# Kernel tuning notes

Hardware: AMD Instinct MI355X
Metric: run time of the kernel (lower is better)

The kernel has to match this reference:

```python
import jax, jax.numpy as jnp
import numpy as np

DIM = 256
HEADS = 4
HEAD_DIM = DIM // HEADS
SCALE = HEAD_DIM ** -0.5


def setup_inputs() -> dict:
    key = jax.random.key(0)
    ks = jax.random.split(key, 6)
    B, N, C = 4, 4096, DIM
    x = jax.random.normal(ks[0], (B, N, C), dtype=jnp.float32)
    # torch.nn.Linear weights are [out, in]; y = x @ W.T (+ b)
    s = 1.0 / np.sqrt(C)
    Wq = jax.random.uniform(ks[1], (C, C), jnp.float32, -s, s)
    Wk = jax.random.uniform(ks[2], (C, C), jnp.float32, -s, s)
    Wv = jax.random.uniform(ks[3], (C, C), jnp.float32, -s, s)
    Wp = jax.random.uniform(ks[4], (C, C), jnp.float32, -s, s)
    bp = jax.random.uniform(ks[5], (C,), jnp.float32, -s, s)
    return {"x": x, "Wq": Wq, "Wk": Wk, "Wv": Wv, "Wp": Wp, "bp": bp}


def reference(x, Wq, Wk, Wv, Wp, bp):
    B, N, C = x.shape
    H, D = HEADS, HEAD_DIM
    # project and split heads: [B, H, N, D]
    def heads(W):
        return (x @ W.T).reshape(B, N, H, D).transpose(0, 2, 1, 3)
    q = heads(Wq)
    k = heads(Wk)
    v = heads(Wv)
    attn = jnp.einsum('bhnd,bhmd->bhnm', q, k) * SCALE  # [B,H,N,N]
    attn = jax.nn.softmax(attn, axis=-1)
    out = jnp.einsum('bhnm,bhmd->bhnd', attn, v)  # [B,H,N,D]
    out = out.transpose(0, 2, 1, 3).reshape(B, N, C)
    return out @ Wp.T + bp
```

## Files before the change

kernel.cpp:

```cpp
#include <hip/hip_runtime.h>

typedef unsigned short u16t;
typedef unsigned int u32t;
typedef __bf16 bf16x8 __attribute__((ext_vector_type(8)));
typedef float f32x4 __attribute__((ext_vector_type(4)));
typedef float f32x16 __attribute__((ext_vector_type(16)));
typedef unsigned int u32x4 __attribute__((ext_vector_type(4)));
typedef unsigned int u32x2 __attribute__((ext_vector_type(2)));

#define DEV static __device__ __forceinline__

DEV u16t f2bf(float f){
  u32t u = __builtin_bit_cast(u32t, f);
  u += 0x7fffu + ((u >> 16) & 1u);
  return (u16t)(u >> 16);
}

DEV u32t cvtpk(float lo, float hi){
  u32t r;
  asm("v_cvt_pk_bf16_f32 %0, %1, %2" : "=v"(r) : "v"(lo), "v"(hi));
  return r;
}

DEV void plswap(u32t &a, u32t &b){
  asm("v_permlane32_swap_b32 %0, %1" : "+v"(a), "+v"(b));
}

DEV float fexp2(float x){
#if __has_builtin(__builtin_amdgcn_exp2f)
  return __builtin_amdgcn_exp2f(x);
#else
  return exp2f(x);
#endif
}

DEV void gll16(const void* g, void* l){
  __builtin_amdgcn_global_load_lds((const __attribute__((address_space(1))) void*)g,
                                   (__attribute__((address_space(3))) void*)l, 16, 0, 0);
}

DEV f32x4 mfma16(bf16x8 a, bf16x8 b, f32x4 c){
  return __builtin_amdgcn_mfma_f32_16x16x32_bf16(a, b, c, 0, 0, 0);
}

DEV f32x16 mfma32(bf16x8 a, bf16x8 b, f32x16 c){
  return __builtin_amdgcn_mfma_f32_32x32x16_bf16(a, b, c, 0, 0, 0);
}

__global__ __launch_bounds__(256) void k_cast_x(const float4* __restrict__ x, u16t* __restrict__ xb){
  int idx = blockIdx.x * 256 + threadIdx.x;
  float4 v = x[idx];
  ushort4 o = make_ushort4(f2bf(v.x), f2bf(v.y), f2bf(v.z), f2bf(v.w));
  *(ushort4*)&xb[idx * 4] = o;
}

__global__ __launch_bounds__(256) void k_cast_w(const float* __restrict__ Wq, const float* __restrict__ Wk,
                         const float* __restrict__ Wv, const float* __restrict__ Wp,
                         u16t* __restrict__ wqkv, u16t* __restrict__ wp){
  int idx = blockIdx.x * 256 + threadIdx.x;
  if (idx < 196608){
    float v;
    if (idx < 65536)        v = Wq[idx] * 0.1803368801f;
    else if (idx < 131072)  v = Wk[idx - 65536];
    else                    v = Wv[idx - 131072];
    wqkv[idx] = f2bf(v);
  } else {
    int j = idx - 196608;
    wp[j] = f2bf(Wp[j]);
  }
}

template<bool IS_QKV>
__global__ __launch_bounds__(256) void k_gemm(const u16t* __restrict__ A, const u16t* __restrict__ W,
    const float* __restrict__ bias, u16t* __restrict__ oq, u16t* __restrict__ okk, u16t* __restrict__ vtg,
    float* __restrict__ op, int Ntot){
  __shared__ u32x4 sm[1536];
  const int tid = threadIdx.x, lane = tid & 63, w = tid >> 6, g = lane >> 4, li = lane & 15;
  const int m0 = blockIdx.x * 128, n0 = blockIdx.y * 64;
  const int wm = w >> 1, wn = w & 1;
  f32x4 acc[4][2] = {};
  for (int kk = 0; kk < 4; ++kk){
    #pragma unroll
    for (int rnd = 0; rnd < 4; ++rnd){
      int cid = rnd * 256 + tid;
      int row = cid >> 3, ch = cid & 7;
      const u16t* src = A + (m0 + row) * 256 + kk * 64 + ((ch ^ (row & 7)) << 3);
      gll16(src, (char*)sm + (rnd * 256 + w * 64) * 16);
    }
    #pragma unroll
    for (int rnd = 0; rnd < 2; ++rnd){
      int cid = rnd * 256 + tid;
      int row = cid >> 3, ch = cid & 7;
      const u16t* src = W + (n0 + row) * 256 + kk * 64 + ((ch ^ (row & 7)) << 3);
      gll16(src, (char*)sm + 16384 + (rnd * 256 + w * 64) * 16);
    }
    __syncthreads();
    #pragma unroll
    for (int ks = 0; ks < 2; ++ks){
      bf16x8 bfr[2];
      #pragma unroll
      for (int nj = 0; nj < 2; ++nj){
        int row = wn * 32 + nj * 16 + li;
        bfr[nj] = __builtin_bit_cast(bf16x8, sm[1024 + row * 8 + ((ks * 4 + g) ^ (row & 7))]);
      }
      #pragma unroll
      for (int mi = 0; mi < 4; ++mi){
        int row = wm * 64 + mi * 16 + li;
        bf16x8 af = __builtin_bit_cast(bf16x8, sm[row * 8 + ((ks * 4 + g) ^ (row & 7))]);
        #pragma unroll
        for (int nj = 0; nj < 2; ++nj)
          acc[mi][nj] = mfma16(af, bfr[nj], acc[mi][nj]);
      }
    }
    __syncthreads();
  }
  if (IS_QKV){
    const int which = n0 >> 8, h = (n0 >> 6) & 3;
    if (which == 2){
      u16t* smv = (u16t*)sm;
      #pragma unroll
      for (int mi = 0; mi < 4; ++mi){
        #pragma unroll
        for (int nj = 0; nj < 2; ++nj){
          int d = wn * 32 + nj * 16 + li;
          int mloc = wm * 64 + mi * 16 + g * 4;
          u32x2 pk2;
          pk2.x = cvtpk(acc[mi][nj][0], acc[mi][nj][1]);
          pk2.y = cvtpk(acc[mi][nj][2], acc[mi][nj][3]);
          int chk = mloc >> 3, inner = (mloc & 7) * 2;
          *(u32x2*)((char*)smv + d * 256 + (((chk ^ (d & 7))) << 4) + inner) = pk2;
        }
      }
      __syncthreads();
      const int b = m0 >> 12, bh2 = b * 4 + h, mbase = m0 & 4095;
      #pragma unroll
      for (int rnd = 0; rnd < 4; ++rnd){
        int qq = rnd * 256 + tid;
        int d = qq & 63, cidx = qq >> 6;
        u32x4 val = *(const u32x4*)((char*)smv + d * 256 + ((cidx ^ (d & 7)) << 4));
        int nt = (mbase >> 6) + (cidx >> 3), i = cidx & 7;
        *(u32x4*)((char*)vtg + ((((size_t)bh2 * 64 + nt) * 8 + i) * 64 + d) * 16) = val;
      }
    } else if (which == 1){
      #pragma unroll
      for (int mi = 0; mi < 4; ++mi){
        int m = m0 + wm * 64 + mi * 16 + g * 4;
        int b = m >> 12;
        #pragma unroll
        for (int nj = 0; nj < 2; ++nj){
          int d = wn * 32 + nj * 16 + li;
          int kk2 = d >> 4, dhi = (d >> 3) & 1, e = d & 7;
          #pragma unroll
          for (int r = 0; r < 4; ++r){
            int row = (m + r) & 4095;
            int nt = row >> 6, jt = (row >> 5) & 1, pp = row & 31;
            okk[(size_t)(b * 4 + h) * 262144 + nt * 4096 + (kk2 * 2 + jt) * 512 + dhi * 256 + pp * 8 + e]
              = f2bf(acc[mi][nj][r]);
          }
        }
      }
    } else {
      #pragma unroll
      for (int mi = 0; mi < 4; ++mi){
        int m = m0 + wm * 64 + mi * 16 + g * 4;
        int b = m >> 12, nn = m & 4095;
        #pragma unroll
        for (int nj = 0; nj < 2; ++nj){
          int d = wn * 32 + nj * 16 + li;
          #pragma unroll
          for (int r = 0; r < 4; ++r)
            oq[((b * 4 + h) * 4096 + nn + r) * 64 + d] = f2bf(acc[mi][nj][r]);
        }
      }
    }
  } else {
    #pragma unroll
    for (int mi = 0; mi < 4; ++mi){
      int m = m0 + wm * 64 + mi * 16 + g * 4;
      #pragma unroll
      for (int nj = 0; nj < 2; ++nj){
        int n = n0 + wn * 32 + nj * 16 + li;
        float bv = bias[n];
        #pragma unroll
        for (int r = 0; r < 4; ++r)
          op[(m + r) * Ntot + n] = acc[mi][nj][r] + bv;
      }
    }
  }
}

__global__ __launch_bounds__(256) void k_flash(const u16t* __restrict__ q,
    const u16t* __restrict__ kslot, const u16t* __restrict__ vslot, u16t* __restrict__ ao){
  __shared__ char sm[32768];
  const int tid = threadIdx.x, lane = tid & 63, w = tid >> 6;
  const int hi = lane >> 5, p = lane & 31;
  const int bid = blockIdx.x;
  const int swz = (bid & 7) * 64 + (bid >> 3);
  const int bh = swz >> 5, qt = swz & 31;
  const int rowbase = qt * 128 + w * 32;
  const char* kbB = (const char*)kslot + (size_t)bh * 524288 + tid * 16;
  const char* vbB = (const char*)vslot + (size_t)bh * 524288 + tid * 16;

  auto stage = [&](int t, int c){
    char* dst = sm + c * 16384 + tid * 16;
    const char* sK = kbB + (size_t)t * 8192;
    const char* sV = vbB + (size_t)t * 8192;
    gll16(sK, dst);
    gll16(sK + 4096, dst + 4096);
    gll16(sV, dst + 8192);
    gll16(sV + 4096, dst + 12288);
  };

  u32x4 qf[4];
  #pragma unroll
  for (int kk = 0; kk < 4; ++kk)
    qf[kk] = *(const u32x4*)&q[((size_t)bh * 4096 + rowbase + p) * 64 + kk * 16 + hi * 8];
  asm volatile("s_waitcnt vmcnt(0)" ::: "memory");
  stage(0, 0);
  stage(1, 1);

  f32x16 ot[2] = {};
  float lsp[4] = {};
  const f32x16 fz = {};

  #pragma unroll 1
  for (int t = 0; t < 64; ++t){
    asm volatile("s_waitcnt vmcnt(4)" ::: "memory");
    __builtin_amdgcn_s_barrier();
    asm volatile("" ::: "memory");
    const char* Kb = sm + (t & 1) * 16384;
    const char* Vt = Kb + 8192;
    f32x16 st[2];
    #pragma unroll
    for (int kk = 0; kk < 4; ++kk)
      #pragma unroll
      for (int jt = 0; jt < 2; ++jt){
        bf16x8 kf = __builtin_bit_cast(bf16x8,
            *(const u32x4*)(Kb + (kk * 2 + jt) * 1024 + lane * 16));
        st[jt] = mfma32(kf, __builtin_bit_cast(bf16x8, qf[kk]), kk == 0 ? fz : st[jt]);
      }
    #pragma unroll
    for (int jt = 0; jt < 2; ++jt){
      float e[16];
      #pragma unroll
      for (int r = 0; r < 16; ++r)
        e[r] = fexp2(st[jt][r]);
      #pragma unroll
      for (int r = 0; r < 16; ++r)
        lsp[r & 3] += e[r];
      u32x4 pf[2];
      #pragma unroll
      for (int s = 0; s < 2; ++s){
        u32t a0 = cvtpk(e[s*8+0], e[s*8+1]);
        u32t a1 = cvtpk(e[s*8+2], e[s*8+3]);
        u32t b0 = cvtpk(e[s*8+4], e[s*8+5]);
        u32t b1 = cvtpk(e[s*8+6], e[s*8+7]);
        plswap(a0, b0);
        plswap(a1, b1);
        pf[s] = (u32x4){a0, a1, b0, b1};
      }
      #pragma unroll
      for (int s = 0; s < 2; ++s)
        #pragma unroll
        for (int dt = 0; dt < 2; ++dt){
          bf16x8 vf = __builtin_bit_cast(bf16x8,
              *(const u32x4*)(Vt + ((jt * 2 + s) * 2 + hi) * 1024 + dt * 512 + p * 16));
          ot[dt] = mfma32(vf, __builtin_bit_cast(bf16x8, pf[s]), ot[dt]);
        }
    }
    asm volatile("s_waitcnt lgkmcnt(0)" ::: "memory");
    __builtin_amdgcn_s_barrier();
    asm volatile("" ::: "memory");
    stage((t + 2) & 63, t & 1);
  }
  asm volatile("s_waitcnt vmcnt(0)" ::: "memory");
  __builtin_amdgcn_s_barrier();
  asm volatile("" ::: "memory");

  float l = (lsp[0] + lsp[1]) + (lsp[2] + lsp[3]);
  l += __shfl_xor(l, 32);
  float inv = __builtin_amdgcn_rcpf(l);

  char* reg = sm + w * 4096;
  #pragma unroll
  for (int dt = 0; dt < 2; ++dt)
    #pragma unroll
    for (int k = 0; k < 8; ++k){
      int d0 = ((2 * k) & 3) + 8 * (k >> 1) + 4 * hi + 32 * dt;
      u32t pkv = cvtpk(ot[dt][2 * k] * inv, ot[dt][2 * k + 1] * inv);
      int ch = d0 >> 3, inner = (d0 & 7) * 2;
      *(u32t*)(reg + p * 128 + ((ch ^ (p & 7)) << 4) + inner) = pkv;
    }
  {
    const int b = bh >> 2, h = bh & 3;
    int row = lane >> 1, half = lane & 1;
    const char* src = sm + w * 4096 + row * 128;
    u16t* dst = ao + ((size_t)b * 4096 + rowbase + row) * 256 + h * 64 + half * 32;
    #pragma unroll
    for (int j = 0; j < 4; ++j){
      int ch = half * 4 + j;
      u32x4 v = *(const u32x4*)(src + ((ch ^ (row & 7)) << 4));
      *(u32x4*)(dst + j * 8) = v;
    }
  }
}

extern "C" void kernel_launch(void* const* d_in, const int* in_sizes, int n_in,
                              void* d_out, int out_size, void* d_ws, size_t ws_size,
                              hipStream_t stream){
  (void)in_sizes; (void)n_in; (void)out_size; (void)ws_size;
  const float* x  = (const float*)d_in[0];
  const float* Wq = (const float*)d_in[1];
  const float* Wk = (const float*)d_in[2];
  const float* Wv = (const float*)d_in[3];
  const float* Wp = (const float*)d_in[4];
  const float* bp = (const float*)d_in[5];
  float* out = (float*)d_out;

  u16t* ws   = (u16t*)d_ws;
  u16t* xb   = ws;
  u16t* qg   = ws + 4194304;
  u16t* kg   = ws + 8388608;
  u16t* vtg  = ws + 12582912;
  u16t* ao   = ws + 16777216;
  u16t* wqkv = ws + 20971520;
  u16t* wpb  = ws + 21168128;

  k_cast_x<<<4096, 256, 0, stream>>>((const float4*)x, xb);
  k_cast_w<<<1024, 256, 0, stream>>>(Wq, Wk, Wv, Wp, wqkv, wpb);
  k_gemm<true><<<dim3(128, 12), 256, 0, stream>>>(xb, wqkv, nullptr, qg, kg, vtg, nullptr, 768);
  k_flash<<<512, 256, 0, stream>>>(qg, kg, vtg, ao);
  k_gemm<false><<<dim3(128, 4), 256, 0, stream>>>(ao, wpb, bp, nullptr, nullptr, nullptr, out, 256);
}
```

Before: 122.1 us.

## Split KV sequence across two wave groups in flash kernel with LDS reduction

Doubles the flash-attention block to 512 threads, with two groups of four waves each processing half of the key/value sequence for the same 128 query rows, each using its own LDS double buffer. Partial outputs and row sums are written to LDS in fp32, summed across the two halves, normalized and packed to bf16 before the store. The aim is more waves in flight per query tile to hide the exp and MFMA latency. In exchange the block needs about 65KB of LDS, which may limit how many blocks fit per CU, and there is an extra combine step. No max-subtraction is needed since the softmax appears to use no running max.

```diff
diff --git a/kernel.cpp b/kernel.cpp
--- a/kernel.cpp
+++ b/kernel.cpp
@@ -189,20 +189,23 @@
   }
 }
 
-__global__ __launch_bounds__(256) void k_flash(const u16t* __restrict__ q,
+__global__ __launch_bounds__(512) void k_flash(const u16t* __restrict__ q,
     const u16t* __restrict__ kslot, const u16t* __restrict__ vslot, u16t* __restrict__ ao){
-  __shared__ char sm[32768];
+  __shared__ char sm[66560];
   const int tid = threadIdx.x, lane = tid & 63, w = tid >> 6;
   const int hi = lane >> 5, p = lane & 31;
+  const int kvh = w >> 2, qg = w & 3;
   const int bid = blockIdx.x;
   const int swz = (bid & 7) * 64 + (bid >> 3);
   const int bh = swz >> 5, qt = swz & 31;
-  const int rowbase = qt * 128 + w * 32;
-  const char* kbB = (const char*)kslot + (size_t)bh * 524288 + tid * 16;
-  const char* vbB = (const char*)vslot + (size_t)bh * 524288 + tid * 16;
+  const int rowbase = qt * 128 + qg * 32;
+  const int r256 = tid & 255;
+  const char* kbB = (const char*)kslot + (size_t)bh * 524288 + (size_t)kvh * 262144 + r256 * 16;
+  const char* vbB = (const char*)vslot + (size_t)bh * 524288 + (size_t)kvh * 262144 + r256 * 16;
+  char* myLds = sm + kvh * 32768;
 
   auto stage = [&](int t, int c){
-    char* dst = sm + c * 16384 + tid * 16;
+    char* dst = myLds + c * 16384 + r256 * 16;
     const char* sK = kbB + (size_t)t * 8192;
     const char* sV = vbB + (size_t)t * 8192;
     gll16(sK, dst);
@@ -224,11 +227,11 @@
   const f32x16 fz = {};
 
   #pragma unroll 1
-  for (int t = 0; t < 64; ++t){
+  for (int t = 0; t < 32; ++t){
     asm volatile("s_waitcnt vmcnt(4)" ::: "memory");
     __builtin_amdgcn_s_barrier();
     asm volatile("" ::: "memory");
-    const char* Kb = sm + (t & 1) * 16384;
+    const char* Kb = myLds + (t & 1) * 16384;
     const char* Vt = Kb + 8192;
     f32x16 st[2];
     #pragma unroll
@@ -271,7 +274,7 @@
     asm volatile("s_waitcnt lgkmcnt(0)" ::: "memory");
     __builtin_amdgcn_s_barrier();
     asm volatile("" ::: "memory");
-    stage((t + 2) & 63, t & 1);
+    stage((t + 2) & 31, t & 1);
   }
   asm volatile("s_waitcnt vmcnt(0)" ::: "memory");
   __builtin_amdgcn_s_barrier();
@@ -279,29 +282,42 @@
 
   float l = (lsp[0] + lsp[1]) + (lsp[2] + lsp[3]);
   l += __shfl_xor(l, 32);
-  float inv = __builtin_amdgcn_rcpf(l);
-
-  char* reg = sm + w * 4096;
-  #pragma unroll
-  for (int dt = 0; dt < 2; ++dt)
-    #pragma unroll
-    for (int k = 0; k < 8; ++k){
-      int d0 = ((2 * k) & 3) + 8 * (k >> 1) + 4 * hi + 32 * dt;
-      u32t pkv = cvtpk(ot[dt][2 * k] * inv, ot[dt][2 * k + 1] * inv);
-      int ch = d0 >> 3, inner = (d0 & 7) * 2;
-      *(u32t*)(reg + p * 128 + ((ch ^ (p & 7)) << 4) + inner) = pkv;
-    }
+  float* lsums = (float*)(sm + 65536);
+  if (lane < 32) lsums[w * 32 + lane] = l;
+
   {
-    const int b = bh >> 2, h = bh & 3;
-    int row = lane >> 1, half = lane & 1;
-    const char* src = sm + w * 4096 + row * 128;
-    u16t* dst = ao + ((size_t)b * 4096 + rowbase + row) * 256 + h * 64 + half * 32;
-    #pragma unroll
-    for (int j = 0; j < 4; ++j){
-      int ch = half * 4 + j;
-      u32x4 v = *(const u32x4*)(src + ((ch ^ (row & 7)) << 4));
-      *(u32x4*)(dst + j * 8) = v;
-    }
+    char* reg = sm + w * 8192;
+    #pragma unroll
+    for (int dt = 0; dt < 2; ++dt)
+      #pragma unroll
+      for (int s4 = 0; s4 < 4; ++s4){
+        f32x4 v4 = {ot[dt][4*s4+0], ot[dt][4*s4+1], ot[dt][4*s4+2], ot[dt][4*s4+3]};
+        int quad = 2 * s4 + hi + 8 * dt;
+        *(f32x4*)(reg + p * 256 + ((quad ^ (p & 15)) << 4)) = v4;
+      }
+  }
+  __syncthreads();
+
+  {
+    const int qrow = tid >> 2, seg = tid & 3;
+    const int qg2 = qrow >> 5, qloc = qrow & 31;
+    float ltot = lsums[qg2 * 32 + qloc] + lsums[(4 + qg2) * 32 + qloc];
+    float inv = __builtin_amdgcn_rcpf(ltot);
+    const int b = bh >> 2, head = bh & 3;
+    u32t pko[8];
+    #pragma unroll
+    for (int k = 0; k < 4; ++k){
+      int quad = seg * 4 + k;
+      int off = qloc * 256 + ((quad ^ (qloc & 15)) << 4);
+      f32x4 s = *(const f32x4*)(sm + qg2 * 8192 + off)
+              + *(const f32x4*)(sm + (4 + qg2) * 8192 + off);
+      s = s * inv;
+      pko[2*k]   = cvtpk(s[0], s[1]);
+      pko[2*k+1] = cvtpk(s[2], s[3]);
+    }
+    u16t* dst = ao + ((size_t)b * 4096 + qt * 128 + qrow) * 256 + head * 64 + seg * 16;
+    *(u32x4*)(dst)     = (u32x4){pko[0], pko[1], pko[2], pko[3]};
+    *(u32x4*)(dst + 8) = (u32x4){pko[4], pko[5], pko[6], pko[7]};
   }
 }
 
@@ -329,6 +345,6 @@
   k_cast_x<<<4096, 256, 0, stream>>>((const float4*)x, xb);
   k_cast_w<<<1024, 256, 0, stream>>>(Wq, Wk, Wv, Wp, wqkv, wpb);
   k_gemm<true><<<dim3(128, 12), 256, 0, stream>>>(xb, wqkv, nullptr, qg, kg, vtg, nullptr, 768);
-  k_flash<<<512, 256, 0, stream>>>(qg, kg, vtg, ao);
+  k_flash<<<512, 512, 0, stream>>>(qg, kg, vtg, ao);
   k_gemm<false><<<dim3(128, 4), 256, 0, stream>>>(ao, wpb, bp, nullptr, nullptr, nullptr, out, 256);
 }
```

Measured after the change: 107.5 us. -12.0%, faster.
